# Optimization experiments

Measured on AMD Instinct MI355X. Metric: run time of the kernel, lower is better.

The kernel has to match this reference:

```python
import jax, jax.numpy as jnp
import numpy as np

N = 100000      # nodes
E = 1600000     # edges
F_IN = 64       # num_node_features
R = 8           # num_relations
G = 256         # graphs in batch
H, C = 4, 32    # GAT heads, per-head channels
NEG_SLOPE_ATT = 0.2    # GATConv attention leaky relu
NEG_SLOPE = 0.01       # F.leaky_relu default


def setup_inputs() -> dict:
    key = jax.random.key(0)
    ks = jax.random.split(key, 12)
    init = lambda k, shape, fan: (jax.random.normal(k, shape, jnp.float32) / np.sqrt(fan).astype(np.float32))
    x = jax.random.normal(ks[0], (N, F_IN), jnp.float32)
    edge_index = jax.random.randint(ks[1], (2, E), 0, N)
    edge_type = jax.random.randint(ks[2], (E,), 0, R)
    batch = (jnp.arange(N) * G) // N  # sorted graph ids, every segment non-empty
    return dict(
        x=x, edge_index=edge_index, edge_type=edge_type, batch=batch,
        gat_w=init(ks[3], (F_IN, H * C), F_IN),
        gat_att_src=init(ks[4], (H, C), C),
        gat_att_dst=init(ks[5], (H, C), C),
        gat_bias=jnp.zeros((H * C,), jnp.float32),
        dense1_w=init(ks[6], (H * C, 16), H * C),
        dense1_b=jnp.zeros((16,), jnp.float32),
        rw1=init(ks[7], (R, F_IN, 32), F_IN),
        root1=init(ks[8], (F_IN, 32), F_IN),
        rb1=jnp.zeros((32,), jnp.float32),
        rw2=init(ks[9], (R, 32, 16), 32),
        root2=init(ks[10], (32, 16), 32),
        rb2=jnp.zeros((16,), jnp.float32),
        dense_w=init(ks[11], (32, 1), 32),
        dense_b=jnp.zeros((1,), jnp.float32),
    )


def _gat(x, src, dst, w, att_src, att_dst, bias):
    h = (x @ w).reshape(N, H, C)                       # [N,H,C]
    a_src = jnp.sum(h * att_src, axis=-1)              # [N,H]
    a_dst = jnp.sum(h * att_dst, axis=-1)              # [N,H]
    e = jax.nn.leaky_relu(a_src[src] + a_dst[dst], NEG_SLOPE_ATT)  # [E,H]
    # segment softmax over incoming edges of each dst node
    m = jax.ops.segment_max(e, dst, num_segments=N)    # [N,H]
    p = jnp.exp(e - m[dst])
    s = jax.ops.segment_sum(p, dst, num_segments=N)    # [N,H]
    alpha = p / s[dst]
    msg = h[src] * alpha[:, :, None]                   # [E,H,C]
    out = jax.ops.segment_sum(msg, dst, num_segments=N)
    return out.reshape(N, H * C) + bias


def _rgcn(x, src, dst, edge_type, w, root, bias):
    # per-relation transform of all nodes, then edge gather (PyG RGCNConv, aggr='mean')
    xw = jnp.einsum('ni,rio->rno', x, w)               # [R,N,out]
    msg = xw[edge_type, src]                           # [E,out]
    comb = dst * R + edge_type                         # mean is per (dst, relation)
    cnt = jax.ops.segment_sum(jnp.ones((E,), x.dtype), comb, num_segments=N * R)
    agg = jax.ops.segment_sum(msg / cnt[comb][:, None], dst, num_segments=N)
    return agg + x @ root + bias


def reference(x, edge_index, edge_type, batch, gat_w, gat_att_src, gat_att_dst,
              gat_bias, dense1_w, dense1_b, rw1, root1, rb1, rw2, root2, rb2,
              dense_w, dense_b):
    src, dst = edge_index[0], edge_index[1]
    # GAT branch (dropout treated as identity / eval mode)
    h = _gat(x, src, dst, gat_w, gat_att_src, gat_att_dst, gat_bias)
    h = jax.nn.leaky_relu(h, NEG_SLOPE)
    h = jax.nn.leaky_relu(h @ dense1_w + dense1_b, NEG_SLOPE)
    gmax = jax.ops.segment_max(h, batch, num_segments=G)          # [G,16]
    # RGCN branch
    z = jax.nn.relu(_rgcn(x, src, dst, edge_type, rw1, root1, rb1))
    z = jax.nn.relu(_rgcn(z, src, dst, edge_type, rw2, root2, rb2))
    nodes_per_graph = jax.ops.segment_sum(jnp.ones((N,), x.dtype), batch, num_segments=G)
    gmean = jax.ops.segment_sum(z, batch, num_segments=G) / nodes_per_graph[:, None]
    # fuse
    zc = jnp.concatenate([gmax, gmean], axis=1)                   # [G,32]
    return zc @ dense_w + dense_b                                  # [G,1]
```

## Files before the change

### kernel.cpp

```cpp
#include <hip/hip_runtime.h>
#include <hip/hip_bf16.h>

typedef __hip_bfloat16 bf16;
typedef unsigned short u16;

#define N_NODES 100000
#define N_EDGES 1600000
#define F_IN 64
#define N_REL 8
#define N_GRAPH 256
#define N_HEAD 4
#define HC 128
#define NBLK_SCAN 391

__device__ __forceinline__ float lrelu(float x, float s) { return x >= 0.f ? x : s * x; }
__device__ __forceinline__ unsigned fenc(float f) {
  unsigned b = __float_as_uint(f);
  return (b & 0x80000000u) ? ~b : (b | 0x80000000u);
}
__device__ __forceinline__ float fdec(unsigned u) {
  float v = __uint_as_float((u & 0x80000000u) ? (u & 0x7fffffffu) : ~u);
  return fmaxf(fminf(v, 3e38f), -3e38f);
}
__device__ __forceinline__ float bf2f(bf16 v) { return __bfloat162float(v); }
__device__ __forceinline__ bf16 f2bf(float v) { return __float2bfloat16(v); }
__device__ __forceinline__ float lo_bf(unsigned u) { return __uint_as_float(u << 16); }
__device__ __forceinline__ float hi_bf(unsigned u) { return __uint_as_float(u & 0xFFFF0000u); }
__device__ __forceinline__ unsigned f2bfu(float v) {
  unsigned u = __float_as_uint(v);
  return (u + 0x7FFFu + ((u >> 16) & 1u)) >> 16;
}

template<bool BF> __device__ __forceinline__ float ldf(const void* p, size_t i) {
  if (BF) { u16 v = ((const u16*)p)[i]; return __uint_as_float(((unsigned)v) << 16); }
  else    { return ((const float*)p)[i]; }
}
template<bool BF> __device__ __forceinline__ float2 ldf2(const void* p, size_t i) {
  if (BF) { unsigned v = ((const unsigned*)p)[i]; return make_float2(lo_bf(v), hi_bf(v)); }
  else    { return ((const float2*)p)[i]; }
}

__global__ void k_probe(const u16* __restrict__ xr, int* __restrict__ flag) {
  int t = threadIdx.x;
  int c = 0;
  for (int i = t; i < 1024; i += 256) {
    unsigned e = (xr[i] >> 7) & 0xFFu;
    if (e >= 100u && e <= 140u) c++;
  }
  __shared__ int sc[256];
  sc[t] = c;
  __syncthreads();
  for (int s = 128; s; s >>= 1) { if (t < s) sc[t] += sc[t + s]; __syncthreads(); }
  if (t == 0) *flag = (sc[0] >= 800) ? 1 : 0;
}

template<bool BF>
__device__ __forceinline__ void gat_h_body(const void* x, const void* w, const void* att_s,
                                           const void* att_d, u16* __restrict__ h,
                                           float* __restrict__ a_src, float* __restrict__ a_dst,
                                           int n, float* xs) {
  int j = threadIdx.x;
  if (j < F_IN) xs[j] = ldf<BF>(x, (size_t)n * F_IN + j);
  __syncthreads();
  float acc = 0.f;
#pragma unroll
  for (int k = 0; k < F_IN; ++k) acc += xs[k] * ldf<BF>(w, (size_t)k * HC + j);
  h[(size_t)n * HC + j] = (u16)f2bfu(acc);
  float ps = acc * ldf<BF>(att_s, j);
  float pd = acc * ldf<BF>(att_d, j);
#pragma unroll
  for (int off = 16; off > 0; off >>= 1) {
    ps += __shfl_down(ps, off, 32);
    pd += __shfl_down(pd, off, 32);
  }
  if ((j & 31) == 0) {
    a_src[n * N_HEAD + (j >> 5)] = ps;
    a_dst[n * N_HEAD + (j >> 5)] = pd;
  }
}

__global__ void k_gath_hist(const void* x, const void* w, const void* att_s, const void* att_d,
                            u16* h, float* a_src, float* a_dst,
                            const int* __restrict__ ei, const int* __restrict__ etype,
                            int* __restrict__ deg, int* __restrict__ cnt, const int* flag) {
  __shared__ float xs[F_IN];
  if (blockIdx.x < N_NODES) {
    if (__builtin_amdgcn_readfirstlane(*flag))
      gat_h_body<true>(x, w, att_s, att_d, h, a_src, a_dst, blockIdx.x, xs);
    else
      gat_h_body<false>(x, w, att_s, att_d, h, a_src, a_dst, blockIdx.x, xs);
  } else {
    int e = (blockIdx.x - N_NODES) * 128 + threadIdx.x;
    if (e < N_EDGES) {
      int d = ei[N_EDGES + e], t = etype[e];
      atomicAdd(&deg[d], 1);
      atomicAdd(&cnt[d * N_REL + t], 1);
    }
  }
}

__global__ void k_scan_a(const int* __restrict__ deg, int* __restrict__ rowptr,
                         int* __restrict__ scanblk) {
  __shared__ int buf[256];
  int tid = threadIdx.x;
  int i = blockIdx.x * 256 + tid;
  int v = (i < N_NODES) ? deg[i] : 0;
  buf[tid] = v;
  __syncthreads();
  for (int st = 1; st < 256; st <<= 1) {
    int t = buf[tid];
    int a = (tid >= st) ? buf[tid - st] : 0;
    __syncthreads();
    buf[tid] = t + a;
    __syncthreads();
  }
  if (i < N_NODES) rowptr[i] = buf[tid] - v;
  if (tid == 255) scanblk[blockIdx.x] = buf[255];
}
__global__ void k_scan_b(int* __restrict__ scanblk) {
  __shared__ int buf[512];
  int tid = threadIdx.x;
  int v = (tid < NBLK_SCAN) ? scanblk[tid] : 0;
  buf[tid] = v;
  __syncthreads();
  for (int st = 1; st < 512; st <<= 1) {
    int t = buf[tid];
    int a = (tid >= st) ? buf[tid - st] : 0;
    __syncthreads();
    buf[tid] = t + a;
    __syncthreads();
  }
  if (tid < NBLK_SCAN) scanblk[tid] = buf[tid] - v;
}
__global__ void k_scan_c(int* __restrict__ rowptr, int* __restrict__ wp,
                         const int* __restrict__ scanblk) {
  int i = blockIdx.x * 256 + threadIdx.x;
  if (i < N_NODES) {
    int val = rowptr[i] + scanblk[blockIdx.x];
    rowptr[i] = val;
    wp[i] = val;
  } else if (i == N_NODES) {
    rowptr[N_NODES] = N_EDGES;
  }
}

__global__ void k_scatter(const int* __restrict__ ei, const int* __restrict__ etype,
                          const float* __restrict__ a_src, const float* __restrict__ a_dst,
                          int* __restrict__ wp, unsigned* __restrict__ csr,
                          float4* __restrict__ p_logit, int* __restrict__ dstarr) {
  int e = blockIdx.x * 256 + threadIdx.x;
  if (e >= N_EDGES) return;
  int sn = ei[e], d = ei[N_EDGES + e], t = etype[e];
  int pos = atomicAdd(&wp[d], 1);
  csr[pos] = (unsigned)sn | ((unsigned)t << 20);
  dstarr[pos] = d;
  const float4 as = *(const float4*)&a_src[sn * 4];
  const float4 ad = *(const float4*)&a_dst[d * 4];
  float4 lg;
  lg.x = lrelu(as.x + ad.x, 0.2f);
  lg.y = lrelu(as.y + ad.y, 0.2f);
  lg.z = lrelu(as.z + ad.z, 0.2f);
  lg.w = lrelu(as.w + ad.w, 0.2f);
  p_logit[pos] = lg;
}

__global__ void k_msum(const int* __restrict__ rowptr, const float* __restrict__ p_logit,
                       float* __restrict__ m_arr, float* __restrict__ si_arr) {
  int tid = threadIdx.x;
  int n = blockIdx.x * 16 + (tid >> 4);
  int l16 = tid & 15, head = l16 & 3, slot = l16 >> 2;
  int base = rowptr[n], deg = rowptr[n + 1] - base;
  float m = -1e30f;
  for (int i = slot; i < deg; i += 4) m = fmaxf(m, p_logit[(size_t)(base + i) * 4 + head]);
  m = fmaxf(m, __shfl_xor(m, 4, 64));
  m = fmaxf(m, __shfl_xor(m, 8, 64));
  float s = 0.f;
  for (int i = slot; i < deg; i += 4) s += __expf(p_logit[(size_t)(base + i) * 4 + head] - m);
  s += __shfl_xor(s, 4, 64);
  s += __shfl_xor(s, 8, 64);
  if (slot == 0) {
    m_arr[n * 4 + head] = m;
    si_arr[n * 4 + head] = (deg > 0) ? 1.f / s : 0.f;
  }
}

__global__ void k_alpha(const int* __restrict__ dstarr, const float* __restrict__ m_arr,
                        const float* __restrict__ si_arr, float4* __restrict__ plog4) {
  int p = blockIdx.x * 256 + threadIdx.x;
  if (p >= N_EDGES) return;
  int d = dstarr[p];
  float4 lg = plog4[p];
  const float4 m4 = *(const float4*)&m_arr[d * 4];
  const float4 s4 = *(const float4*)&si_arr[d * 4];
  float4 a;
  a.x = __expf(lg.x - m4.x) * s4.x;
  a.y = __expf(lg.y - m4.y) * s4.y;
  a.z = __expf(lg.z - m4.z) * s4.z;
  a.w = __expf(lg.w - m4.w) * s4.w;
  plog4[p] = a;
}

template<bool BF>
__device__ __forceinline__ void gat_agg_body(const int* __restrict__ rowptr,
                                             const unsigned* __restrict__ csr,
                                             const float* __restrict__ alpha,
                                             const uint2* __restrict__ hu2, const void* gbias,
                                             const void* d1w, const void* d1b,
                                             const int* __restrict__ batch,
                                             unsigned* __restrict__ gmax, int* __restrict__ npg,
                                             float (*os)[132], int bid) {
  int tid = threadIdx.x;
  int wave = tid >> 6, l = tid & 63;
  int d = bid * 4 + wave;
  int base = rowptr[d];
  int deg = rowptr[d + 1] - base;
  int slot = l >> 5, cl = l & 31;
  int head = cl >> 3;
  float a0 = 0.f, a1 = 0.f, a2 = 0.f, a3 = 0.f;
  int i = slot;
  for (; i + 6 < deg; i += 8) {
    unsigned sp0 = csr[base + i],     sp1 = csr[base + i + 2];
    unsigned sp2 = csr[base + i + 4], sp3 = csr[base + i + 6];
    float av0 = alpha[(size_t)(base + i) * 4 + head];
    float av1 = alpha[(size_t)(base + i + 2) * 4 + head];
    float av2 = alpha[(size_t)(base + i + 4) * 4 + head];
    float av3 = alpha[(size_t)(base + i + 6) * 4 + head];
    uint2 h0 = hu2[(size_t)(sp0 & 0xFFFFF) * 32 + cl];
    uint2 h1 = hu2[(size_t)(sp1 & 0xFFFFF) * 32 + cl];
    uint2 h2 = hu2[(size_t)(sp2 & 0xFFFFF) * 32 + cl];
    uint2 h3 = hu2[(size_t)(sp3 & 0xFFFFF) * 32 + cl];
    a0 += lo_bf(h0.x) * av0 + lo_bf(h1.x) * av1 + lo_bf(h2.x) * av2 + lo_bf(h3.x) * av3;
    a1 += hi_bf(h0.x) * av0 + hi_bf(h1.x) * av1 + hi_bf(h2.x) * av2 + hi_bf(h3.x) * av3;
    a2 += lo_bf(h0.y) * av0 + lo_bf(h1.y) * av1 + lo_bf(h2.y) * av2 + lo_bf(h3.y) * av3;
    a3 += hi_bf(h0.y) * av0 + hi_bf(h1.y) * av1 + hi_bf(h2.y) * av2 + hi_bf(h3.y) * av3;
  }
  for (; i < deg; i += 2) {
    unsigned sp = csr[base + i];
    float av = alpha[(size_t)(base + i) * 4 + head];
    uint2 hv = hu2[(size_t)(sp & 0xFFFFF) * 32 + cl];
    a0 += lo_bf(hv.x) * av;
    a1 += hi_bf(hv.x) * av;
    a2 += lo_bf(hv.y) * av;
    a3 += hi_bf(hv.y) * av;
  }
  a0 += __shfl_xor(a0, 32, 64);
  a1 += __shfl_xor(a1, 32, 64);
  a2 += __shfl_xor(a2, 32, 64);
  a3 += __shfl_xor(a3, 32, 64);
  if (slot == 0) {
    os[wave][4 * cl + 0] = lrelu(a0 + ldf<BF>(gbias, 4 * cl + 0), 0.01f);
    os[wave][4 * cl + 1] = lrelu(a1 + ldf<BF>(gbias, 4 * cl + 1), 0.01f);
    os[wave][4 * cl + 2] = lrelu(a2 + ldf<BF>(gbias, 4 * cl + 2), 0.01f);
    os[wave][4 * cl + 3] = lrelu(a3 + ldf<BF>(gbias, 4 * cl + 3), 0.01f);
  }
  __syncthreads();
  if (tid < 64) {
    int node = tid >> 4, out = tid & 15;
    float acc = ldf<BF>(d1b, out);
#pragma unroll
    for (int k = 0; k < HC; ++k) acc += os[node][k] * ldf<BF>(d1w, (size_t)k * 16 + out);
    acc = lrelu(acc, 0.01f);
    atomicMax(&gmax[batch[bid * 4 + node] * 16 + out], fenc(acc));
  }
  if (tid < 4) atomicAdd(&npg[batch[bid * 4 + tid]], 1);
}

template<bool BF>
__device__ __forceinline__ void xw1_body(const void* x, const void* rw1, bf16* __restrict__ xw1,
                                         int n0, int r, float (*xs)[F_IN]) {
  int tid = threadIdx.x;
  for (int i = tid; i < 8 * F_IN; i += 256) {
    int nn = n0 + (i >> 6);
    xs[i >> 6][i & 63] = (nn < N_NODES) ? ldf<BF>(x, (size_t)nn * F_IN + (i & 63)) : 0.f;
  }
  __syncthreads();
  int nl = tid >> 5, c = tid & 31;
  int n = n0 + nl;
  float acc = 0.f;
#pragma unroll
  for (int k = 0; k < F_IN; ++k) acc += xs[nl][k] * ldf<BF>(rw1, (size_t)(r * F_IN + k) * 32 + c);
  if (n < N_NODES) xw1[((size_t)r * N_NODES + n) * 32 + c] = f2bf(acc);
}

__global__ void k_aggxw1(const int* rowptr, const unsigned* csr, const float* alpha,
                         const u16* h, const void* gbias, const void* d1w, const void* d1b,
                         const int* batch, unsigned* gmax, int* npg,
                         const void* x, const void* rw1, bf16* xw1, const int* flag) {
  __shared__ float sh[544];
  int bf = __builtin_amdgcn_readfirstlane(*flag);
  if (blockIdx.x < 25000) {
    if (bf) gat_agg_body<true>(rowptr, csr, alpha, (const uint2*)h, gbias, d1w, d1b,
                               batch, gmax, npg, (float(*)[132])sh, blockIdx.x);
    else    gat_agg_body<false>(rowptr, csr, alpha, (const uint2*)h, gbias, d1w, d1b,
                                batch, gmax, npg, (float(*)[132])sh, blockIdx.x);
  } else {
    int nb = blockIdx.x - 25000;
    int n0 = (nb % 12500) * 8;
    int r  = nb / 12500;
    if (bf) xw1_body<true>(x, rw1, xw1, n0, r, (float(*)[F_IN])sh);
    else    xw1_body<false>(x, rw1, xw1, n0, r, (float(*)[F_IN])sh);
  }
}

template<bool BF>
__device__ __forceinline__ void ragg1_body(const int* __restrict__ rowptr,
                                           const unsigned* __restrict__ csr,
                                           const int* __restrict__ cnt,
                                           const unsigned* __restrict__ xw, const void* x,
                                           const void* root1, const void* rb1,
                                           float* __restrict__ z1) {
  __shared__ float xs[4][F_IN];
  __shared__ float cinv[4][N_REL];
  int tid = threadIdx.x;
  int n0 = blockIdx.x * 4;
  {
    int nn = n0 + (tid >> 6);
    xs[tid >> 6][tid & 63] = ldf<BF>(x, (size_t)nn * F_IN + (tid & 63));
  }
  if (tid < 32) {
    int cv = cnt[(n0 + (tid >> 3)) * N_REL + (tid & 7)];
    cinv[tid >> 3][tid & 7] = (cv > 0) ? 1.f / (float)cv : 0.f;
  }
  __syncthreads();
  int wave = tid >> 6, l = tid & 63;
  int slot = l >> 4, cl = l & 15;
  int n = n0 + wave;
  int base = rowptr[n], deg = rowptr[n + 1] - base;
  float a0 = 0.f, a1 = 0.f;
  int i = slot;
  for (; i + 4 < deg; i += 8) {
    unsigned sp0 = csr[base + i], sp1 = csr[base + i + 4];
    int t0 = sp0 >> 20, t1 = sp1 >> 20;
    unsigned v0 = xw[((size_t)t0 * N_NODES + (sp0 & 0xFFFFF)) * 16 + cl];
    unsigned v1 = xw[((size_t)t1 * N_NODES + (sp1 & 0xFFFFF)) * 16 + cl];
    float c0 = cinv[wave][t0], c1 = cinv[wave][t1];
    a0 += lo_bf(v0) * c0 + lo_bf(v1) * c1;
    a1 += hi_bf(v0) * c0 + hi_bf(v1) * c1;
  }
  if (i < deg) {
    unsigned sp = csr[base + i];
    int t = sp >> 20;
    unsigned v = xw[((size_t)t * N_NODES + (sp & 0xFFFFF)) * 16 + cl];
    float c0 = cinv[wave][t];
    a0 += lo_bf(v) * c0;
    a1 += hi_bf(v) * c0;
  }
#pragma unroll
  for (int kk = 0; kk < 16; ++kk) {
    int k = slot * 16 + kk;
    float xv = xs[wave][k];
    float2 wv = ldf2<BF>(root1, (size_t)k * 16 + cl);
    a0 += xv * wv.x;
    a1 += xv * wv.y;
  }
  a0 += __shfl_xor(a0, 16, 64); a0 += __shfl_xor(a0, 32, 64);
  a1 += __shfl_xor(a1, 16, 64); a1 += __shfl_xor(a1, 32, 64);
  if (slot == 0) {
    z1[(size_t)n * 32 + 2 * cl]     = fmaxf(a0 + ldf<BF>(rb1, 2 * cl), 0.f);
    z1[(size_t)n * 32 + 2 * cl + 1] = fmaxf(a1 + ldf<BF>(rb1, 2 * cl + 1), 0.f);
  }
}
__global__ void k_ragg1(const int* rowptr, const unsigned* csr, const int* cnt,
                        const bf16* xw1, const void* x, const void* root1, const void* rb1,
                        float* z1, const int* flag) {
  if (__builtin_amdgcn_readfirstlane(*flag))
    ragg1_body<true>(rowptr, csr, cnt, (const unsigned*)xw1, x, root1, rb1, z1);
  else
    ragg1_body<false>(rowptr, csr, cnt, (const unsigned*)xw1, x, root1, rb1, z1);
}

template<bool BF>
__device__ __forceinline__ void zw2_body(const float* __restrict__ z1, const void* rw2,
                                         bf16* __restrict__ zw2) {
  __shared__ float zs[16][32];
  int tid = threadIdx.x;
  int n0 = blockIdx.x * 16;
  for (int i = tid; i < 16 * 32; i += 256) {
    int nn = n0 + (i >> 5);
    zs[i >> 5][i & 31] = (nn < N_NODES) ? z1[(size_t)nn * 32 + (i & 31)] : 0.f;
  }
  __syncthreads();
  int nl = tid >> 4, c = tid & 15;
  int n = n0 + nl, r = blockIdx.y;
  float acc = 0.f;
#pragma unroll
  for (int k = 0; k < 32; ++k) acc += zs[nl][k] * ldf<BF>(rw2, (size_t)(r * 32 + k) * 16 + c);
  if (n < N_NODES) zw2[((size_t)r * N_NODES + n) * 16 + c] = f2bf(acc);
}
__global__ void k_zw2(const float* z1, const void* rw2, bf16* zw2, const int* flag) {
  if (__builtin_amdgcn_readfirstlane(*flag)) zw2_body<true>(z1, rw2, zw2);
  else zw2_body<false>(z1, rw2, zw2);
}

template<bool BF>
__device__ __forceinline__ void ragg2_body(const int* __restrict__ rowptr,
                                           const unsigned* __restrict__ csr,
                                           const int* __restrict__ cnt,
                                           const unsigned* __restrict__ zw,
                                           const float* __restrict__ z1, const void* root2,
                                           const void* rb2, const int* __restrict__ batch,
                                           float* __restrict__ gsum) {
  __shared__ float zs[4][33];
  __shared__ float cinv[4][N_REL];
  int tid = threadIdx.x;
  int n0 = blockIdx.x * 4;
  if (tid < 128) {
    int nn = n0 + (tid >> 5);
    zs[tid >> 5][tid & 31] = z1[(size_t)nn * 32 + (tid & 31)];
  }
  if (tid < 32) {
    int cv = cnt[(n0 + (tid >> 3)) * N_REL + (tid & 7)];
    cinv[tid >> 3][tid & 7] = (cv > 0) ? 1.f / (float)cv : 0.f;
  }
  __syncthreads();
  int wave = tid >> 6, l = tid & 63;
  int slot = l >> 3, cl = l & 7;
  int n = n0 + wave;
  int base = rowptr[n], deg = rowptr[n + 1] - base;
  float a0 = 0.f, a1 = 0.f;
  int i = slot;
  for (; i + 8 < deg; i += 16) {
    unsigned sp0 = csr[base + i], sp1 = csr[base + i + 8];
    int t0 = sp0 >> 20, t1 = sp1 >> 20;
    unsigned v0 = zw[((size_t)t0 * N_NODES + (sp0 & 0xFFFFF)) * 8 + cl];
    unsigned v1 = zw[((size_t)t1 * N_NODES + (sp1 & 0xFFFFF)) * 8 + cl];
    float c0 = cinv[wave][t0], c1 = cinv[wave][t1];
    a0 += lo_bf(v0) * c0 + lo_bf(v1) * c1;
    a1 += hi_bf(v0) * c0 + hi_bf(v1) * c1;
  }
  if (i < deg) {
    unsigned sp = csr[base + i];
    int t = sp >> 20;
    unsigned v = zw[((size_t)t * N_NODES + (sp & 0xFFFFF)) * 8 + cl];
    float c0 = cinv[wave][t];
    a0 += lo_bf(v) * c0;
    a1 += hi_bf(v) * c0;
  }
#pragma unroll
  for (int kk = 0; kk < 4; ++kk) {
    int k = slot * 4 + kk;
    float zv = zs[wave][k];
    float2 wv = ldf2<BF>(root2, (size_t)k * 8 + cl);
    a0 += zv * wv.x;
    a1 += zv * wv.y;
  }
  a0 += __shfl_xor(a0, 8, 64); a0 += __shfl_xor(a0, 16, 64); a0 += __shfl_xor(a0, 32, 64);
  a1 += __shfl_xor(a1, 8, 64); a1 += __shfl_xor(a1, 16, 64); a1 += __shfl_xor(a1, 32, 64);
  if (slot == 0) {
    float z2a = fmaxf(a0 + ldf<BF>(rb2, 2 * cl), 0.f);
    float z2b = fmaxf(a1 + ldf<BF>(rb2, 2 * cl + 1), 0.f);
    int g = batch[n];
    atomicAdd(&gsum[g * 16 + 2 * cl], z2a);
    atomicAdd(&gsum[g * 16 + 2 * cl + 1], z2b);
  }
}
__global__ void k_ragg2(const int* rowptr, const unsigned* csr, const int* cnt,
                        const bf16* zw2, const float* z1, const void* root2, const void* rb2,
                        const int* batch, float* gsum, const int* flag) {
  if (__builtin_amdgcn_readfirstlane(*flag))
    ragg2_body<true>(rowptr, csr, cnt, (const unsigned*)zw2, z1, root2, rb2, batch, gsum);
  else
    ragg2_body<false>(rowptr, csr, cnt, (const unsigned*)zw2, z1, root2, rb2, batch, gsum);
}

template<bool BF>
__device__ __forceinline__ void final_body(const unsigned* __restrict__ gmax,
                                           const float* __restrict__ gsum,
                                           const int* __restrict__ npg, const void* dw,
                                           const void* db, void* out) {
  int g = threadIdx.x;
  if (g >= N_GRAPH) return;
  float acc = ldf<BF>(db, 0);
  int np = npg[g]; if (np < 1) np = 1;
  float inv = 1.f / (float)np;
#pragma unroll
  for (int c = 0; c < 16; ++c) {
    acc += fdec(gmax[g * 16 + c]) * ldf<BF>(dw, c);
    acc += (gsum[g * 16 + c] * inv) * ldf<BF>(dw, 16 + c);
  }
  if (BF) ((bf16*)out)[g] = f2bf(acc);
  else ((float*)out)[g] = acc;
}
__global__ void k_final(const unsigned* gmax, const float* gsum, const int* npg,
                        const void* dw, const void* db, void* out, const int* flag) {
  if (__builtin_amdgcn_readfirstlane(*flag)) final_body<true>(gmax, gsum, npg, dw, db, out);
  else final_body<false>(gmax, gsum, npg, dw, db, out);
}

extern "C" void kernel_launch(void* const* d_in, const int* in_sizes, int n_in,
                              void* d_out, int out_size, void* d_ws, size_t ws_size,
                              hipStream_t stream) {
  const void* x        = d_in[0];
  const int*  ei       = (const int*)d_in[1];
  const int*  etype    = (const int*)d_in[2];
  const int*  batch    = (const int*)d_in[3];
  const void* gat_w    = d_in[4];
  const void* att_src  = d_in[5];
  const void* att_dst  = d_in[6];
  const void* gat_bias = d_in[7];
  const void* d1w      = d_in[8];
  const void* d1b      = d_in[9];
  const void* rw1      = d_in[10];
  const void* root1    = d_in[11];
  const void* rb1      = d_in[12];
  const void* rw2      = d_in[13];
  const void* root2    = d_in[14];
  const void* rb2      = d_in[15];
  const void* dw       = d_in[16];
  const void* db       = d_in[17];

  char* ws = (char*)d_ws;
  const size_t o_h     = 0;
  const size_t o_plog  = 25600000;
  const size_t o_xw1   = 51200000;
  const size_t o_dst   = 51200000;
  const size_t o_zw2   = 0;
  const size_t o_asrc  = 102400000;
  const size_t o_adst  = 104000000;
  const size_t o_deg   = 105600000;
  const size_t o_rowp  = 106000000;
  const size_t o_wp    = 106400016;
  const size_t o_cnt   = 106800016;
  const size_t o_csr   = 110000016;
  const size_t o_z1    = 116400016;
  const size_t o_sblk  = 129200016;
  const size_t o_gmax  = 129201600;
  const size_t o_gsum  = 129217984;
  const size_t o_npg   = 129234368;
  const size_t o_flag  = 129235392;
  const size_t total   = 129235396;
  if (ws_size < total) return;

  u16*      h      = (u16*)(ws + o_h);
  float*    plog   = (float*)(ws + o_plog);
  bf16*     xw1    = (bf16*)(ws + o_xw1);
  int*      dstarr = (int*)(ws + o_dst);
  bf16*     zw2    = (bf16*)(ws + o_zw2);
  float*    a_src  = (float*)(ws + o_asrc);
  float*    a_dst  = (float*)(ws + o_adst);
  int*      deg    = (int*)(ws + o_deg);
  int*      rowptr = (int*)(ws + o_rowp);
  int*      wp     = (int*)(ws + o_wp);
  int*      cnt    = (int*)(ws + o_cnt);
  unsigned* csr    = (unsigned*)(ws + o_csr);
  float*    z1     = (float*)(ws + o_z1);
  int*      sblk   = (int*)(ws + o_sblk);
  unsigned* gmax   = (unsigned*)(ws + o_gmax);
  float*    gsum   = (float*)(ws + o_gsum);
  int*      npg    = (int*)(ws + o_npg);
  int*      flag   = (int*)(ws + o_flag);

  k_probe<<<1, 256, 0, stream>>>((const u16*)x, flag);

  hipMemsetAsync(ws + o_deg, 0, o_csr - o_deg, stream);
  hipMemsetAsync(ws + o_gmax, 0, 33792, stream);

  k_gath_hist<<<N_NODES + 12500, 128, 0, stream>>>(x, gat_w, att_src, att_dst, h, a_src, a_dst,
                                                   ei, etype, deg, cnt, flag);

  k_scan_a<<<NBLK_SCAN, 256, 0, stream>>>(deg, rowptr, sblk);
  k_scan_b<<<1, 512, 0, stream>>>(sblk);
  k_scan_c<<<NBLK_SCAN, 256, 0, stream>>>(rowptr, wp, sblk);
  k_scatter<<<(N_EDGES + 255) / 256, 256, 0, stream>>>(ei, etype, a_src, a_dst, wp, csr,
                                                       (float4*)plog, dstarr);

  k_msum<<<N_NODES / 16, 256, 0, stream>>>(rowptr, plog, a_src, a_dst);
  k_alpha<<<(N_EDGES + 255) / 256, 256, 0, stream>>>(dstarr, a_src, a_dst, (float4*)plog);

  k_aggxw1<<<25000 + 100000, 256, 0, stream>>>(rowptr, csr, plog, h, gat_bias, d1w, d1b,
                                               batch, gmax, npg, x, rw1, xw1, flag);

  k_ragg1<<<N_NODES / 4, 256, 0, stream>>>(rowptr, csr, cnt, xw1, x, root1, rb1, z1, flag);

  k_zw2<<<dim3((N_NODES + 15) / 16, N_REL), 256, 0, stream>>>(z1, rw2, zw2, flag);
  k_ragg2<<<N_NODES / 4, 256, 0, stream>>>(rowptr, csr, cnt, zw2, z1, root2, rb2,
                                           batch, gsum, flag);

  k_final<<<1, 256, 0, stream>>>(gmax, gsum, npg, dw, db, d_out, flag);
}
```

Before: 1.230 ms.

## Store GAT features in channel-planar layout and logits per head for cache-blocked aggregation

The GAT node features are written in 8 planes of 16 channels each, and edge logits/alphas are stored as one array per head instead of interleaved float4. The GAT aggregation kernel now walks each node's incoming edges once per plane, gathering 32-byte rows from a 3.2 MB plane that should stay resident in L2, instead of 256-byte rows from the full 25.6 MB feature table. The fused GAT-aggregate and xw1 kernel is split into two separate launches. In exchange, csr and alpha are re-read 8 times per node, there are more shuffle reductions, and each narrow gather may use cache lines less efficiently.

```diff
diff --git a/kernel.cpp b/kernel.cpp
--- a/kernel.cpp
+++ b/kernel.cpp
@@ -56,7 +56,7 @@
 
 template<bool BF>
 __device__ __forceinline__ void gat_h_body(const void* x, const void* w, const void* att_s,
-                                           const void* att_d, u16* __restrict__ h,
+                                           const void* att_d, u16* __restrict__ hpl,
                                            float* __restrict__ a_src, float* __restrict__ a_dst,
                                            int n, float* xs) {
   int j = threadIdx.x;
@@ -65,7 +65,7 @@
   float acc = 0.f;
 #pragma unroll
   for (int k = 0; k < F_IN; ++k) acc += xs[k] * ldf<BF>(w, (size_t)k * HC + j);
-  h[(size_t)n * HC + j] = (u16)f2bfu(acc);
+  hpl[((size_t)(j >> 4) * N_NODES + n) * 16 + (j & 15)] = (u16)f2bfu(acc);
   float ps = acc * ldf<BF>(att_s, j);
   float pd = acc * ldf<BF>(att_d, j);
 #pragma unroll
@@ -80,15 +80,15 @@
 }
 
 __global__ void k_gath_hist(const void* x, const void* w, const void* att_s, const void* att_d,
-                            u16* h, float* a_src, float* a_dst,
+                            u16* hpl, float* a_src, float* a_dst,
                             const int* __restrict__ ei, const int* __restrict__ etype,
                             int* __restrict__ deg, int* __restrict__ cnt, const int* flag) {
   __shared__ float xs[F_IN];
   if (blockIdx.x < N_NODES) {
     if (__builtin_amdgcn_readfirstlane(*flag))
-      gat_h_body<true>(x, w, att_s, att_d, h, a_src, a_dst, blockIdx.x, xs);
+      gat_h_body<true>(x, w, att_s, att_d, hpl, a_src, a_dst, blockIdx.x, xs);
     else
-      gat_h_body<false>(x, w, att_s, att_d, h, a_src, a_dst, blockIdx.x, xs);
+      gat_h_body<false>(x, w, att_s, att_d, hpl, a_src, a_dst, blockIdx.x, xs);
   } else {
     int e = (blockIdx.x - N_NODES) * 128 + threadIdx.x;
     if (e < N_EDGES) {
@@ -147,7 +147,7 @@
 __global__ void k_scatter(const int* __restrict__ ei, const int* __restrict__ etype,
                           const float* __restrict__ a_src, const float* __restrict__ a_dst,
                           int* __restrict__ wp, unsigned* __restrict__ csr,
-                          float4* __restrict__ p_logit, int* __restrict__ dstarr) {
+                          float* __restrict__ asoa, int* __restrict__ dstarr) {
   int e = blockIdx.x * 256 + threadIdx.x;
   if (e >= N_EDGES) return;
   int sn = ei[e], d = ei[N_EDGES + e], t = etype[e];
@@ -156,26 +156,25 @@
   dstarr[pos] = d;
   const float4 as = *(const float4*)&a_src[sn * 4];
   const float4 ad = *(const float4*)&a_dst[d * 4];
-  float4 lg;
-  lg.x = lrelu(as.x + ad.x, 0.2f);
-  lg.y = lrelu(as.y + ad.y, 0.2f);
-  lg.z = lrelu(as.z + ad.z, 0.2f);
-  lg.w = lrelu(as.w + ad.w, 0.2f);
-  p_logit[pos] = lg;
-}
-
-__global__ void k_msum(const int* __restrict__ rowptr, const float* __restrict__ p_logit,
+  asoa[0 * N_EDGES + pos] = lrelu(as.x + ad.x, 0.2f);
+  asoa[1 * N_EDGES + pos] = lrelu(as.y + ad.y, 0.2f);
+  asoa[2 * N_EDGES + pos] = lrelu(as.z + ad.z, 0.2f);
+  asoa[3 * N_EDGES + pos] = lrelu(as.w + ad.w, 0.2f);
+}
+
+__global__ void k_msum(const int* __restrict__ rowptr, const float* __restrict__ asoa,
                        float* __restrict__ m_arr, float* __restrict__ si_arr) {
   int tid = threadIdx.x;
   int n = blockIdx.x * 16 + (tid >> 4);
   int l16 = tid & 15, head = l16 & 3, slot = l16 >> 2;
   int base = rowptr[n], deg = rowptr[n + 1] - base;
+  const float* ap = asoa + (size_t)head * N_EDGES;
   float m = -1e30f;
-  for (int i = slot; i < deg; i += 4) m = fmaxf(m, p_logit[(size_t)(base + i) * 4 + head]);
+  for (int i = slot; i < deg; i += 4) m = fmaxf(m, ap[base + i]);
   m = fmaxf(m, __shfl_xor(m, 4, 64));
   m = fmaxf(m, __shfl_xor(m, 8, 64));
   float s = 0.f;
-  for (int i = slot; i < deg; i += 4) s += __expf(p_logit[(size_t)(base + i) * 4 + head] - m);
+  for (int i = slot; i < deg; i += 4) s += __expf(ap[base + i] - m);
   s += __shfl_xor(s, 4, 64);
   s += __shfl_xor(s, 8, 64);
   if (slot == 0) {
@@ -185,73 +184,60 @@
 }
 
 __global__ void k_alpha(const int* __restrict__ dstarr, const float* __restrict__ m_arr,
-                        const float* __restrict__ si_arr, float4* __restrict__ plog4) {
+                        const float* __restrict__ si_arr, float* __restrict__ asoa) {
   int p = blockIdx.x * 256 + threadIdx.x;
   if (p >= N_EDGES) return;
   int d = dstarr[p];
-  float4 lg = plog4[p];
   const float4 m4 = *(const float4*)&m_arr[d * 4];
   const float4 s4 = *(const float4*)&si_arr[d * 4];
-  float4 a;
-  a.x = __expf(lg.x - m4.x) * s4.x;
-  a.y = __expf(lg.y - m4.y) * s4.y;
-  a.z = __expf(lg.z - m4.z) * s4.z;
-  a.w = __expf(lg.w - m4.w) * s4.w;
-  plog4[p] = a;
+  asoa[0 * N_EDGES + p] = __expf(asoa[0 * N_EDGES + p] - m4.x) * s4.x;
+  asoa[1 * N_EDGES + p] = __expf(asoa[1 * N_EDGES + p] - m4.y) * s4.y;
+  asoa[2 * N_EDGES + p] = __expf(asoa[2 * N_EDGES + p] - m4.z) * s4.z;
+  asoa[3 * N_EDGES + p] = __expf(asoa[3 * N_EDGES + p] - m4.w) * s4.w;
 }
 
 template<bool BF>
 __device__ __forceinline__ void gat_agg_body(const int* __restrict__ rowptr,
                                              const unsigned* __restrict__ csr,
-                                             const float* __restrict__ alpha,
-                                             const uint2* __restrict__ hu2, const void* gbias,
+                                             const float* __restrict__ asoa,
+                                             const unsigned* __restrict__ hpl, const void* gbias,
                                              const void* d1w, const void* d1b,
                                              const int* __restrict__ batch,
                                              unsigned* __restrict__ gmax, int* __restrict__ npg,
-                                             float (*os)[132], int bid) {
+                                             float (*os)[132]) {
   int tid = threadIdx.x;
   int wave = tid >> 6, l = tid & 63;
-  int d = bid * 4 + wave;
+  int d = blockIdx.x * 4 + wave;
   int base = rowptr[d];
   int deg = rowptr[d + 1] - base;
-  int slot = l >> 5, cl = l & 31;
-  int head = cl >> 3;
-  float a0 = 0.f, a1 = 0.f, a2 = 0.f, a3 = 0.f;
-  int i = slot;
-  for (; i + 6 < deg; i += 8) {
-    unsigned sp0 = csr[base + i],     sp1 = csr[base + i + 2];
-    unsigned sp2 = csr[base + i + 4], sp3 = csr[base + i + 6];
-    float av0 = alpha[(size_t)(base + i) * 4 + head];
-    float av1 = alpha[(size_t)(base + i + 2) * 4 + head];
-    float av2 = alpha[(size_t)(base + i + 4) * 4 + head];
-    float av3 = alpha[(size_t)(base + i + 6) * 4 + head];
-    uint2 h0 = hu2[(size_t)(sp0 & 0xFFFFF) * 32 + cl];
-    uint2 h1 = hu2[(size_t)(sp1 & 0xFFFFF) * 32 + cl];
-    uint2 h2 = hu2[(size_t)(sp2 & 0xFFFFF) * 32 + cl];
-    uint2 h3 = hu2[(size_t)(sp3 & 0xFFFFF) * 32 + cl];
-    a0 += lo_bf(h0.x) * av0 + lo_bf(h1.x) * av1 + lo_bf(h2.x) * av2 + lo_bf(h3.x) * av3;
-    a1 += hi_bf(h0.x) * av0 + hi_bf(h1.x) * av1 + hi_bf(h2.x) * av2 + hi_bf(h3.x) * av3;
-    a2 += lo_bf(h0.y) * av0 + lo_bf(h1.y) * av1 + lo_bf(h2.y) * av2 + lo_bf(h3.y) * av3;
-    a3 += hi_bf(h0.y) * av0 + hi_bf(h1.y) * av1 + hi_bf(h2.y) * av2 + hi_bf(h3.y) * av3;
-  }
-  for (; i < deg; i += 2) {
-    unsigned sp = csr[base + i];
-    float av = alpha[(size_t)(base + i) * 4 + head];
-    uint2 hv = hu2[(size_t)(sp & 0xFFFFF) * 32 + cl];
-    a0 += lo_bf(hv.x) * av;
-    a1 += hi_bf(hv.x) * av;
-    a2 += lo_bf(hv.y) * av;
-    a3 += hi_bf(hv.y) * av;
-  }
-  a0 += __shfl_xor(a0, 32, 64);
-  a1 += __shfl_xor(a1, 32, 64);
-  a2 += __shfl_xor(a2, 32, 64);
-  a3 += __shfl_xor(a3, 32, 64);
-  if (slot == 0) {
-    os[wave][4 * cl + 0] = lrelu(a0 + ldf<BF>(gbias, 4 * cl + 0), 0.01f);
-    os[wave][4 * cl + 1] = lrelu(a1 + ldf<BF>(gbias, 4 * cl + 1), 0.01f);
-    os[wave][4 * cl + 2] = lrelu(a2 + ldf<BF>(gbias, 4 * cl + 2), 0.01f);
-    os[wave][4 * cl + 3] = lrelu(a3 + ldf<BF>(gbias, 4 * cl + 3), 0.01f);
+  int slot = l >> 3, cl = l & 7;
+#pragma unroll
+  for (int ph = 0; ph < 8; ++ph) {
+    const float* ap = asoa + (size_t)(ph >> 1) * N_EDGES;
+    const unsigned* hp = hpl + (size_t)ph * (N_NODES * 8);
+    float a0 = 0.f, a1 = 0.f;
+    int i = slot;
+    for (; i + 8 < deg; i += 16) {
+      unsigned sp0 = csr[base + i], sp1 = csr[base + i + 8];
+      float av0 = ap[base + i], av1 = ap[base + i + 8];
+      unsigned v0 = hp[(size_t)(sp0 & 0xFFFFF) * 8 + cl];
+      unsigned v1 = hp[(size_t)(sp1 & 0xFFFFF) * 8 + cl];
+      a0 += lo_bf(v0) * av0 + lo_bf(v1) * av1;
+      a1 += hi_bf(v0) * av0 + hi_bf(v1) * av1;
+    }
+    if (i < deg) {
+      unsigned sp = csr[base + i];
+      float av = ap[base + i];
+      unsigned v = hp[(size_t)(sp & 0xFFFFF) * 8 + cl];
+      a0 += lo_bf(v) * av;
+      a1 += hi_bf(v) * av;
+    }
+    a0 += __shfl_xor(a0, 8, 64); a0 += __shfl_xor(a0, 16, 64); a0 += __shfl_xor(a0, 32, 64);
+    a1 += __shfl_xor(a1, 8, 64); a1 += __shfl_xor(a1, 16, 64); a1 += __shfl_xor(a1, 32, 64);
+    if (slot == 0) {
+      os[wave][ph * 16 + 2 * cl]     = lrelu(a0 + ldf<BF>(gbias, ph * 16 + 2 * cl), 0.01f);
+      os[wave][ph * 16 + 2 * cl + 1] = lrelu(a1 + ldf<BF>(gbias, ph * 16 + 2 * cl + 1), 0.01f);
+    }
   }
   __syncthreads();
   if (tid < 64) {
@@ -260,9 +246,20 @@
 #pragma unroll
     for (int k = 0; k < HC; ++k) acc += os[node][k] * ldf<BF>(d1w, (size_t)k * 16 + out);
     acc = lrelu(acc, 0.01f);
-    atomicMax(&gmax[batch[bid * 4 + node] * 16 + out], fenc(acc));
-  }
-  if (tid < 4) atomicAdd(&npg[batch[bid * 4 + tid]], 1);
+    atomicMax(&gmax[batch[blockIdx.x * 4 + node] * 16 + out], fenc(acc));
+  }
+  if (tid < 4) atomicAdd(&npg[batch[blockIdx.x * 4 + tid]], 1);
+}
+__global__ void k_gat_agg(const int* rowptr, const unsigned* csr, const float* asoa,
+                          const u16* hpl, const void* gbias, const void* d1w, const void* d1b,
+                          const int* batch, unsigned* gmax, int* npg, const int* flag) {
+  __shared__ float os[4][132];
+  if (__builtin_amdgcn_readfirstlane(*flag))
+    gat_agg_body<true>(rowptr, csr, asoa, (const unsigned*)hpl, gbias, d1w, d1b,
+                       batch, gmax, npg, os);
+  else
+    gat_agg_body<false>(rowptr, csr, asoa, (const unsigned*)hpl, gbias, d1w, d1b,
+                        batch, gmax, npg, os);
 }
 
 template<bool BF>
@@ -281,25 +278,11 @@
   for (int k = 0; k < F_IN; ++k) acc += xs[nl][k] * ldf<BF>(rw1, (size_t)(r * F_IN + k) * 32 + c);
   if (n < N_NODES) xw1[((size_t)r * N_NODES + n) * 32 + c] = f2bf(acc);
 }
-
-__global__ void k_aggxw1(const int* rowptr, const unsigned* csr, const float* alpha,
-                         const u16* h, const void* gbias, const void* d1w, const void* d1b,
-                         const int* batch, unsigned* gmax, int* npg,
-                         const void* x, const void* rw1, bf16* xw1, const int* flag) {
-  __shared__ float sh[544];
-  int bf = __builtin_amdgcn_readfirstlane(*flag);
-  if (blockIdx.x < 25000) {
-    if (bf) gat_agg_body<true>(rowptr, csr, alpha, (const uint2*)h, gbias, d1w, d1b,
-                               batch, gmax, npg, (float(*)[132])sh, blockIdx.x);
-    else    gat_agg_body<false>(rowptr, csr, alpha, (const uint2*)h, gbias, d1w, d1b,
-                                batch, gmax, npg, (float(*)[132])sh, blockIdx.x);
-  } else {
-    int nb = blockIdx.x - 25000;
-    int n0 = (nb % 12500) * 8;
-    int r  = nb / 12500;
-    if (bf) xw1_body<true>(x, rw1, xw1, n0, r, (float(*)[F_IN])sh);
-    else    xw1_body<false>(x, rw1, xw1, n0, r, (float(*)[F_IN])sh);
-  }
+__global__ void k_xw1(const void* x, const void* rw1, bf16* xw1, const int* flag) {
+  __shared__ float xs[8][F_IN];
+  int n0 = blockIdx.x * 8, r = blockIdx.y;
+  if (__builtin_amdgcn_readfirstlane(*flag)) xw1_body<true>(x, rw1, xw1, n0, r, xs);
+  else xw1_body<false>(x, rw1, xw1, n0, r, xs);
 }
 
 template<bool BF>
@@ -511,7 +494,7 @@
 
   char* ws = (char*)d_ws;
   const size_t o_h     = 0;
-  const size_t o_plog  = 25600000;
+  const size_t o_asoa  = 25600000;
   const size_t o_xw1   = 51200000;
   const size_t o_dst   = 51200000;
   const size_t o_zw2   = 0;
@@ -531,8 +514,8 @@
   const size_t total   = 129235396;
   if (ws_size < total) return;
 
-  u16*      h      = (u16*)(ws + o_h);
-  float*    plog   = (float*)(ws + o_plog);
+  u16*      hpl    = (u16*)(ws + o_h);
+  float*    asoa   = (float*)(ws + o_asoa);
   bf16*     xw1    = (bf16*)(ws + o_xw1);
   int*      dstarr = (int*)(ws + o_dst);
   bf16*     zw2    = (bf16*)(ws + o_zw2);
@@ -555,21 +538,22 @@
   hipMemsetAsync(ws + o_deg, 0, o_csr - o_deg, stream);
   hipMemsetAsync(ws + o_gmax, 0, 33792, stream);
 
-  k_gath_hist<<<N_NODES + 12500, 128, 0, stream>>>(x, gat_w, att_src, att_dst, h, a_src, a_dst,
-                                                   ei, etype, deg, cnt, flag);
+  k_gath_hist<<<N_NODES + 12500, 128, 0, stream>>>(x, gat_w, att_src, att_dst, hpl,
+                                                   a_src, a_dst, ei, etype, deg, cnt, flag);
 
   k_scan_a<<<NBLK_SCAN, 256, 0, stream>>>(deg, rowptr, sblk);
   k_scan_b<<<1, 512, 0, stream>>>(sblk);
   k_scan_c<<<NBLK_SCAN, 256, 0, stream>>>(rowptr, wp, sblk);
   k_scatter<<<(N_EDGES + 255) / 256, 256, 0, stream>>>(ei, etype, a_src, a_dst, wp, csr,
-                                                       (float4*)plog, dstarr);
-
-  k_msum<<<N_NODES / 16, 256, 0, stream>>>(rowptr, plog, a_src, a_dst);
-  k_alpha<<<(N_EDGES + 255) / 256, 256, 0, stream>>>(dstarr, a_src, a_dst, (float4*)plog);
-
-  k_aggxw1<<<25000 + 100000, 256, 0, stream>>>(rowptr, csr, plog, h, gat_bias, d1w, d1b,
-                                               batch, gmax, npg, x, rw1, xw1, flag);
-
+                                                       asoa, dstarr);
+
+  k_msum<<<N_NODES / 16, 256, 0, stream>>>(rowptr, asoa, a_src, a_dst);
+  k_alpha<<<(N_EDGES + 255) / 256, 256, 0, stream>>>(dstarr, a_src, a_dst, asoa);
+
+  k_gat_agg<<<N_NODES / 4, 256, 0, stream>>>(rowptr, csr, asoa, hpl, gat_bias, d1w, d1b,
+                                             batch, gmax, npg, flag);
+
+  k_xw1<<<dim3((N_NODES + 7) / 8, N_REL), 256, 0, stream>>>(x, rw1, xw1, flag);
   k_ragg1<<<N_NODES / 4, 256, 0, stream>>>(rowptr, csr, cnt, xw1, x, root1, rb1, z1, flag);
 
   k_zw2<<<dim3((N_NODES + 15) / 16, N_REL), 256, 0, stream>>>(z1, rw2, zw2, flag);
```

New measurement: 1.599 ms. +30.0%, slower.

## Fuse softmax normalization into GAT aggregation, batch 4 nodes per GAT-h block

Applied to the files above, without the earlier changes.

Removes the separate k_alpha pass and the dstarr array. The GAT aggregation now computes exp(logit - max) * inv_sum inline from per-node max and inverse-sum values, which saves one full edge-sized read and write plus the dst index traffic. The GAT-h kernel now processes 4 nodes per block, reusing each weight load across 4 accumulators and cutting block count 4x. The combined aggregation/xw1 kernel is split back into two separate launches, which adds a launch and drops the overlap the shared grid gave.

```diff
diff --git a/kernel.cpp b/kernel.cpp
--- a/kernel.cpp
+++ b/kernel.cpp
@@ -22,10 +22,9 @@
   float v = __uint_as_float((u & 0x80000000u) ? (u & 0x7fffffffu) : ~u);
   return fmaxf(fminf(v, 3e38f), -3e38f);
 }
-__device__ __forceinline__ float bf2f(bf16 v) { return __bfloat162float(v); }
-__device__ __forceinline__ bf16 f2bf(float v) { return __float2bfloat16(v); }
 __device__ __forceinline__ float lo_bf(unsigned u) { return __uint_as_float(u << 16); }
 __device__ __forceinline__ float hi_bf(unsigned u) { return __uint_as_float(u & 0xFFFF0000u); }
+__device__ __forceinline__ bf16 f2bf(float v) { return __float2bfloat16(v); }
 __device__ __forceinline__ unsigned f2bfu(float v) {
   unsigned u = __float_as_uint(v);
   return (u + 0x7FFFu + ((u >> 16) & 1u)) >> 16;
@@ -58,24 +57,36 @@
 __device__ __forceinline__ void gat_h_body(const void* x, const void* w, const void* att_s,
                                            const void* att_d, u16* __restrict__ h,
                                            float* __restrict__ a_src, float* __restrict__ a_dst,
-                                           int n, float* xs) {
-  int j = threadIdx.x;
-  if (j < F_IN) xs[j] = ldf<BF>(x, (size_t)n * F_IN + j);
-  __syncthreads();
-  float acc = 0.f;
-#pragma unroll
-  for (int k = 0; k < F_IN; ++k) acc += xs[k] * ldf<BF>(w, (size_t)k * HC + j);
-  h[(size_t)n * HC + j] = (u16)f2bfu(acc);
-  float ps = acc * ldf<BF>(att_s, j);
-  float pd = acc * ldf<BF>(att_d, j);
-#pragma unroll
-  for (int off = 16; off > 0; off >>= 1) {
-    ps += __shfl_down(ps, off, 32);
-    pd += __shfl_down(pd, off, 32);
-  }
-  if ((j & 31) == 0) {
-    a_src[n * N_HEAD + (j >> 5)] = ps;
-    a_dst[n * N_HEAD + (j >> 5)] = pd;
+                                           int n0, float (*xs)[F_IN]) {
+  int tid = threadIdx.x;
+  for (int i = tid; i < 4 * F_IN; i += 128)
+    xs[i >> 6][i & 63] = ldf<BF>(x, (size_t)(n0 + (i >> 6)) * F_IN + (i & 63));
+  __syncthreads();
+  int j = tid;
+  float acc0 = 0.f, acc1 = 0.f, acc2 = 0.f, acc3 = 0.f;
+#pragma unroll
+  for (int k = 0; k < F_IN; ++k) {
+    float wf = ldf<BF>(w, (size_t)k * HC + j);
+    acc0 += xs[0][k] * wf;
+    acc1 += xs[1][k] * wf;
+    acc2 += xs[2][k] * wf;
+    acc3 += xs[3][k] * wf;
+  }
+  float asj = ldf<BF>(att_s, j), adj = ldf<BF>(att_d, j);
+  float accs[4] = {acc0, acc1, acc2, acc3};
+#pragma unroll
+  for (int q = 0; q < 4; ++q) {
+    h[(size_t)(n0 + q) * HC + j] = (u16)f2bfu(accs[q]);
+    float ps = accs[q] * asj, pd = accs[q] * adj;
+#pragma unroll
+    for (int off = 16; off > 0; off >>= 1) {
+      ps += __shfl_down(ps, off, 32);
+      pd += __shfl_down(pd, off, 32);
+    }
+    if ((j & 31) == 0) {
+      a_src[(n0 + q) * N_HEAD + (j >> 5)] = ps;
+      a_dst[(n0 + q) * N_HEAD + (j >> 5)] = pd;
+    }
   }
 }
 
@@ -83,14 +94,14 @@
                             u16* h, float* a_src, float* a_dst,
                             const int* __restrict__ ei, const int* __restrict__ etype,
                             int* __restrict__ deg, int* __restrict__ cnt, const int* flag) {
-  __shared__ float xs[F_IN];
-  if (blockIdx.x < N_NODES) {
+  __shared__ float xs[4][F_IN];
+  if (blockIdx.x < 25000) {
     if (__builtin_amdgcn_readfirstlane(*flag))
-      gat_h_body<true>(x, w, att_s, att_d, h, a_src, a_dst, blockIdx.x, xs);
+      gat_h_body<true>(x, w, att_s, att_d, h, a_src, a_dst, blockIdx.x * 4, xs);
     else
-      gat_h_body<false>(x, w, att_s, att_d, h, a_src, a_dst, blockIdx.x, xs);
+      gat_h_body<false>(x, w, att_s, att_d, h, a_src, a_dst, blockIdx.x * 4, xs);
   } else {
-    int e = (blockIdx.x - N_NODES) * 128 + threadIdx.x;
+    int e = (blockIdx.x - 25000) * 128 + threadIdx.x;
     if (e < N_EDGES) {
       int d = ei[N_EDGES + e], t = etype[e];
       atomicAdd(&deg[d], 1);
@@ -147,13 +158,12 @@
 __global__ void k_scatter(const int* __restrict__ ei, const int* __restrict__ etype,
                           const float* __restrict__ a_src, const float* __restrict__ a_dst,
                           int* __restrict__ wp, unsigned* __restrict__ csr,
-                          float4* __restrict__ p_logit, int* __restrict__ dstarr) {
+                          float4* __restrict__ p_logit) {
   int e = blockIdx.x * 256 + threadIdx.x;
   if (e >= N_EDGES) return;
   int sn = ei[e], d = ei[N_EDGES + e], t = etype[e];
   int pos = atomicAdd(&wp[d], 1);
   csr[pos] = (unsigned)sn | ((unsigned)t << 20);
-  dstarr[pos] = d;
   const float4 as = *(const float4*)&a_src[sn * 4];
   const float4 ad = *(const float4*)&a_dst[d * 4];
   float4 lg;
@@ -184,47 +194,35 @@
   }
 }
 
-__global__ void k_alpha(const int* __restrict__ dstarr, const float* __restrict__ m_arr,
-                        const float* __restrict__ si_arr, float4* __restrict__ plog4) {
-  int p = blockIdx.x * 256 + threadIdx.x;
-  if (p >= N_EDGES) return;
-  int d = dstarr[p];
-  float4 lg = plog4[p];
-  const float4 m4 = *(const float4*)&m_arr[d * 4];
-  const float4 s4 = *(const float4*)&si_arr[d * 4];
-  float4 a;
-  a.x = __expf(lg.x - m4.x) * s4.x;
-  a.y = __expf(lg.y - m4.y) * s4.y;
-  a.z = __expf(lg.z - m4.z) * s4.z;
-  a.w = __expf(lg.w - m4.w) * s4.w;
-  plog4[p] = a;
-}
-
 template<bool BF>
 __device__ __forceinline__ void gat_agg_body(const int* __restrict__ rowptr,
                                              const unsigned* __restrict__ csr,
-                                             const float* __restrict__ alpha,
+                                             const float* __restrict__ lg,
+                                             const float* __restrict__ m_arr,
+                                             const float* __restrict__ si_arr,
                                              const uint2* __restrict__ hu2, const void* gbias,
                                              const void* d1w, const void* d1b,
                                              const int* __restrict__ batch,
                                              unsigned* __restrict__ gmax, int* __restrict__ npg,
-                                             float (*os)[132], int bid) {
+                                             float (*os)[132]) {
   int tid = threadIdx.x;
   int wave = tid >> 6, l = tid & 63;
-  int d = bid * 4 + wave;
+  int d = blockIdx.x * 4 + wave;
   int base = rowptr[d];
   int deg = rowptr[d + 1] - base;
   int slot = l >> 5, cl = l & 31;
   int head = cl >> 3;
+  float m = m_arr[d * 4 + head];
+  float si = si_arr[d * 4 + head];
   float a0 = 0.f, a1 = 0.f, a2 = 0.f, a3 = 0.f;
   int i = slot;
   for (; i + 6 < deg; i += 8) {
     unsigned sp0 = csr[base + i],     sp1 = csr[base + i + 2];
     unsigned sp2 = csr[base + i + 4], sp3 = csr[base + i + 6];
-    float av0 = alpha[(size_t)(base + i) * 4 + head];
-    float av1 = alpha[(size_t)(base + i + 2) * 4 + head];
-    float av2 = alpha[(size_t)(base + i + 4) * 4 + head];
-    float av3 = alpha[(size_t)(base + i + 6) * 4 + head];
+    float av0 = __expf(lg[(size_t)(base + i) * 4 + head] - m) * si;
+    float av1 = __expf(lg[(size_t)(base + i + 2) * 4 + head] - m) * si;
+    float av2 = __expf(lg[(size_t)(base + i + 4) * 4 + head] - m) * si;
+    float av3 = __expf(lg[(size_t)(base + i + 6) * 4 + head] - m) * si;
     uint2 h0 = hu2[(size_t)(sp0 & 0xFFFFF) * 32 + cl];
     uint2 h1 = hu2[(size_t)(sp1 & 0xFFFFF) * 32 + cl];
     uint2 h2 = hu2[(size_t)(sp2 & 0xFFFFF) * 32 + cl];
@@ -236,7 +234,7 @@
   }
   for (; i < deg; i += 2) {
     unsigned sp = csr[base + i];
-    float av = alpha[(size_t)(base + i) * 4 + head];
+    float av = __expf(lg[(size_t)(base + i) * 4 + head] - m) * si;
     uint2 hv = hu2[(size_t)(sp & 0xFFFFF) * 32 + cl];
     a0 += lo_bf(hv.x) * av;
     a1 += hi_bf(hv.x) * av;
@@ -260,9 +258,21 @@
 #pragma unroll
     for (int k = 0; k < HC; ++k) acc += os[node][k] * ldf<BF>(d1w, (size_t)k * 16 + out);
     acc = lrelu(acc, 0.01f);
-    atomicMax(&gmax[batch[bid * 4 + node] * 16 + out], fenc(acc));
-  }
-  if (tid < 4) atomicAdd(&npg[batch[bid * 4 + tid]], 1);
+    atomicMax(&gmax[batch[blockIdx.x * 4 + node] * 16 + out], fenc(acc));
+  }
+  if (tid < 4) atomicAdd(&npg[batch[blockIdx.x * 4 + tid]], 1);
+}
+__global__ void k_gat_agg(const int* rowptr, const unsigned* csr, const float* lg,
+                          const float* m_arr, const float* si_arr,
+                          const u16* h, const void* gbias, const void* d1w, const void* d1b,
+                          const int* batch, unsigned* gmax, int* npg, const int* flag) {
+  __shared__ float os[4][132];
+  if (__builtin_amdgcn_readfirstlane(*flag))
+    gat_agg_body<true>(rowptr, csr, lg, m_arr, si_arr, (const uint2*)h, gbias, d1w, d1b,
+                       batch, gmax, npg, os);
+  else
+    gat_agg_body<false>(rowptr, csr, lg, m_arr, si_arr, (const uint2*)h, gbias, d1w, d1b,
+                        batch, gmax, npg, os);
 }
 
 template<bool BF>
@@ -281,25 +291,11 @@
   for (int k = 0; k < F_IN; ++k) acc += xs[nl][k] * ldf<BF>(rw1, (size_t)(r * F_IN + k) * 32 + c);
   if (n < N_NODES) xw1[((size_t)r * N_NODES + n) * 32 + c] = f2bf(acc);
 }
-
-__global__ void k_aggxw1(const int* rowptr, const unsigned* csr, const float* alpha,
-                         const u16* h, const void* gbias, const void* d1w, const void* d1b,
-                         const int* batch, unsigned* gmax, int* npg,
-                         const void* x, const void* rw1, bf16* xw1, const int* flag) {
-  __shared__ float sh[544];
-  int bf = __builtin_amdgcn_readfirstlane(*flag);
-  if (blockIdx.x < 25000) {
-    if (bf) gat_agg_body<true>(rowptr, csr, alpha, (const uint2*)h, gbias, d1w, d1b,
-                               batch, gmax, npg, (float(*)[132])sh, blockIdx.x);
-    else    gat_agg_body<false>(rowptr, csr, alpha, (const uint2*)h, gbias, d1w, d1b,
-                                batch, gmax, npg, (float(*)[132])sh, blockIdx.x);
-  } else {
-    int nb = blockIdx.x - 25000;
-    int n0 = (nb % 12500) * 8;
-    int r  = nb / 12500;
-    if (bf) xw1_body<true>(x, rw1, xw1, n0, r, (float(*)[F_IN])sh);
-    else    xw1_body<false>(x, rw1, xw1, n0, r, (float(*)[F_IN])sh);
-  }
+__global__ void k_xw1(const void* x, const void* rw1, bf16* xw1, const int* flag) {
+  __shared__ float xs[8][F_IN];
+  int n0 = blockIdx.x * 8, r = blockIdx.y;
+  if (__builtin_amdgcn_readfirstlane(*flag)) xw1_body<true>(x, rw1, xw1, n0, r, xs);
+  else xw1_body<false>(x, rw1, xw1, n0, r, xs);
 }
 
 template<bool BF>
@@ -308,9 +304,8 @@
                                            const int* __restrict__ cnt,
                                            const unsigned* __restrict__ xw, const void* x,
                                            const void* root1, const void* rb1,
-                                           float* __restrict__ z1) {
-  __shared__ float xs[4][F_IN];
-  __shared__ float cinv[4][N_REL];
+                                           float* __restrict__ z1,
+                                           float (*xs)[F_IN], float (*cinv)[N_REL]) {
   int tid = threadIdx.x;
   int n0 = blockIdx.x * 4;
   {
@@ -363,16 +358,17 @@
 __global__ void k_ragg1(const int* rowptr, const unsigned* csr, const int* cnt,
                         const bf16* xw1, const void* x, const void* root1, const void* rb1,
                         float* z1, const int* flag) {
+  __shared__ float xs[4][F_IN];
+  __shared__ float cinv[4][N_REL];
   if (__builtin_amdgcn_readfirstlane(*flag))
-    ragg1_body<true>(rowptr, csr, cnt, (const unsigned*)xw1, x, root1, rb1, z1);
+    ragg1_body<true>(rowptr, csr, cnt, (const unsigned*)xw1, x, root1, rb1, z1, xs, cinv);
   else
-    ragg1_body<false>(rowptr, csr, cnt, (const unsigned*)xw1, x, root1, rb1, z1);
+    ragg1_body<false>(rowptr, csr, cnt, (const unsigned*)xw1, x, root1, rb1, z1, xs, cinv);
 }
 
 template<bool BF>
 __device__ __forceinline__ void zw2_body(const float* __restrict__ z1, const void* rw2,
-                                         bf16* __restrict__ zw2) {
-  __shared__ float zs[16][32];
+                                         bf16* __restrict__ zw2, float (*zs)[32]) {
   int tid = threadIdx.x;
   int n0 = blockIdx.x * 16;
   for (int i = tid; i < 16 * 32; i += 256) {
@@ -388,8 +384,9 @@
   if (n < N_NODES) zw2[((size_t)r * N_NODES + n) * 16 + c] = f2bf(acc);
 }
 __global__ void k_zw2(const float* z1, const void* rw2, bf16* zw2, const int* flag) {
-  if (__builtin_amdgcn_readfirstlane(*flag)) zw2_body<true>(z1, rw2, zw2);
-  else zw2_body<false>(z1, rw2, zw2);
+  __shared__ float zs[16][32];
+  if (__builtin_amdgcn_readfirstlane(*flag)) zw2_body<true>(z1, rw2, zw2, zs);
+  else zw2_body<false>(z1, rw2, zw2, zs);
 }
 
 template<bool BF>
@@ -399,9 +396,8 @@
                                            const unsigned* __restrict__ zw,
                                            const float* __restrict__ z1, const void* root2,
                                            const void* rb2, const int* __restrict__ batch,
-                                           float* __restrict__ gsum) {
-  __shared__ float zs[4][33];
-  __shared__ float cinv[4][N_REL];
+                                           float* __restrict__ gsum,
+                                           float (*zs)[33], float (*cinv)[N_REL]) {
   int tid = threadIdx.x;
   int n0 = blockIdx.x * 4;
   if (tid < 128) {
@@ -457,10 +453,14 @@
 __global__ void k_ragg2(const int* rowptr, const unsigned* csr, const int* cnt,
                         const bf16* zw2, const float* z1, const void* root2, const void* rb2,
                         const int* batch, float* gsum, const int* flag) {
+  __shared__ float zs[4][33];
+  __shared__ float cinv[4][N_REL];
   if (__builtin_amdgcn_readfirstlane(*flag))
-    ragg2_body<true>(rowptr, csr, cnt, (const unsigned*)zw2, z1, root2, rb2, batch, gsum);
+    ragg2_body<true>(rowptr, csr, cnt, (const unsigned*)zw2, z1, root2, rb2, batch, gsum,
+                     zs, cinv);
   else
-    ragg2_body<false>(rowptr, csr, cnt, (const unsigned*)zw2, z1, root2, rb2, batch, gsum);
+    ragg2_body<false>(rowptr, csr, cnt, (const unsigned*)zw2, z1, root2, rb2, batch, gsum,
+                      zs, cinv);
 }
 
 template<bool BF>
@@ -513,7 +513,6 @@
   const size_t o_h     = 0;
   const size_t o_plog  = 25600000;
   const size_t o_xw1   = 51200000;
-  const size_t o_dst   = 51200000;
   const size_t o_zw2   = 0;
   const size_t o_asrc  = 102400000;
   const size_t o_adst  = 104000000;
@@ -534,7 +533,6 @@
   u16*      h      = (u16*)(ws + o_h);
   float*    plog   = (float*)(ws + o_plog);
   bf16*     xw1    = (bf16*)(ws + o_xw1);
-  int*      dstarr = (int*)(ws + o_dst);
   bf16*     zw2    = (bf16*)(ws + o_zw2);
   float*    a_src  = (float*)(ws + o_asrc);
   float*    a_dst  = (float*)(ws + o_adst);
@@ -555,21 +553,21 @@
   hipMemsetAsync(ws + o_deg, 0, o_csr - o_deg, stream);
   hipMemsetAsync(ws + o_gmax, 0, 33792, stream);
 
-  k_gath_hist<<<N_NODES + 12500, 128, 0, stream>>>(x, gat_w, att_src, att_dst, h, a_src, a_dst,
-                                                   ei, etype, deg, cnt, flag);
+  k_gath_hist<<<25000 + 12500, 128, 0, stream>>>(x, gat_w, att_src, att_dst, h,
+                                                 a_src, a_dst, ei, etype, deg, cnt, flag);
 
   k_scan_a<<<NBLK_SCAN, 256, 0, stream>>>(deg, rowptr, sblk);
   k_scan_b<<<1, 512, 0, stream>>>(sblk);
   k_scan_c<<<NBLK_SCAN, 256, 0, stream>>>(rowptr, wp, sblk);
   k_scatter<<<(N_EDGES + 255) / 256, 256, 0, stream>>>(ei, etype, a_src, a_dst, wp, csr,
-                                                       (float4*)plog, dstarr);
+                                                       (float4*)plog);
 
   k_msum<<<N_NODES / 16, 256, 0, stream>>>(rowptr, plog, a_src, a_dst);
-  k_alpha<<<(N_EDGES + 255) / 256, 256, 0, stream>>>(dstarr, a_src, a_dst, (float4*)plog);
-
-  k_aggxw1<<<25000 + 100000, 256, 0, stream>>>(rowptr, csr, plog, h, gat_bias, d1w, d1b,
-                                               batch, gmax, npg, x, rw1, xw1, flag);
-
+
+  k_gat_agg<<<N_NODES / 4, 256, 0, stream>>>(rowptr, csr, plog, a_src, a_dst, h, gat_bias,
+                                             d1w, d1b, batch, gmax, npg, flag);
+
+  k_xw1<<<dim3((N_NODES + 7) / 8, N_REL), 256, 0, stream>>>(x, rw1, xw1, flag);
   k_ragg1<<<N_NODES / 4, 256, 0, stream>>>(rowptr, csr, cnt, xw1, x, root1, rb1, z1, flag);
 
   k_zw2<<<dim3((N_NODES + 15) / 16, N_REL), 256, 0, stream>>>(z1, rw2, zw2, flag);
```

New measurement: 1.837 ms. 1.49x slower.
